# Kernel optimization log

Hardware: AMD Instinct MI355X
Metric: run time of the kernel (lower is better)

The kernel has to match this reference:

```python
import jax, jax.numpy as jnp
import numpy as np

B, N, C, HEADS, R = 8, 4096, 256, 8, 4  # N = H*W, R = reduction_ratio
LN_EPS = 1e-5


def setup_inputs() -> dict:
    key = jax.random.key(0)
    ks = jax.random.split(key, 6)
    sc = 0.02
    return {
        "x": jax.random.normal(ks[0], (B, N, C), jnp.float32),
        "conv_w": jax.random.normal(ks[1], (C, C, R, R), jnp.float32) * sc,  # OIHW
        "conv_b": jnp.zeros((C,), jnp.float32),
        "ln_g": jnp.ones((C,), jnp.float32),
        "ln_b": jnp.zeros((C,), jnp.float32),
        "kv_w": jax.random.normal(ks[2], (2 * C, C), jnp.float32) * sc,  # torch Linear (out,in)
        "kv_b": jnp.zeros((2 * C,), jnp.float32),
        "q_w": jax.random.normal(ks[3], (C, C), jnp.float32) * sc,
        "q_b": jnp.zeros((C,), jnp.float32),
        "out_w": jax.random.normal(ks[4], (C, C), jnp.float32) * sc,
        "out_b": jnp.zeros((C,), jnp.float32),
        "H": 64,
        "W": 64,
    }


def reference(x, conv_w, conv_b, ln_g, ln_b, kv_w, kv_b, q_w, q_b, out_w, out_b, H, W):
    Bz, Nq, Ch = x.shape
    d = Ch // HEADS
    scale = 1.0 / np.sqrt(float(d)).astype(np.float32)

    # spatial reduction: (B,N,C) -> (B,C,H,W) -> strided conv -> (B, M, C)
    x1 = x.transpose(0, 2, 1).reshape(Bz, Ch, H, W)
    x1 = jax.lax.conv_general_dilated(
        x1, conv_w, window_strides=(R, R), padding="VALID",
        dimension_numbers=("NCHW", "OIHW", "NCHW"))
    x1 = x1 + conv_b[None, :, None, None]
    x1 = x1.reshape(Bz, Ch, -1).transpose(0, 2, 1)  # (B, M, C), M=(H/R)*(W/R)

    # LayerNorm over channels
    mu = x1.mean(-1, keepdims=True)
    var = x1.var(-1, keepdims=True)
    x1 = (x1 - mu) / jnp.sqrt(var + LN_EPS) * ln_g + ln_b

    # K,V from reduced tokens
    kv = x1 @ kv_w.T + kv_b                                  # (B, M, 2C)
    M = kv.shape[1]
    kv = kv.reshape(Bz, M, 2, HEADS, d).transpose(2, 0, 3, 1, 4)  # (2,B,h,M,d)
    k, v = kv[0], kv[1]

    # Q from full-resolution tokens
    q = (x @ q_w.T + q_b).reshape(Bz, Nq, HEADS, d).transpose(0, 2, 1, 3)  # (B,h,N,d)

    attn = jax.nn.softmax(jnp.einsum("bhnd,bhmd->bhnm", q, k) * scale, axis=-1)
    out = jnp.einsum("bhnm,bhmd->bhnd", attn, v)             # (B,h,N,d)
    out = out.transpose(0, 2, 1, 3).reshape(Bz, Nq, Ch)
    return out @ out_w.T + out_b
```

## Files before the change

### kernel.cpp

```cpp
#include <hip/hip_runtime.h>
#include <math.h>

#define LN_EPS 1e-5f
#define SCALE_QK 0.17677669529663687f

using bf16x8 = __bf16 __attribute__((ext_vector_type(8)));
using f32x4 = float __attribute__((ext_vector_type(4)));

__device__ __forceinline__ ushort f2bf(float f) {
  unsigned u = __float_as_uint(f);
  u += 0x7fff + ((u >> 16) & 1);
  return (ushort)(u >> 16);
}

__device__ __forceinline__ void gload_lds16(const ushort* g, ushort* l) {
  __builtin_amdgcn_global_load_lds((__attribute__((address_space(1))) void*)g,
                                   (__attribute__((address_space(3))) void*)l, 16, 0, 0);
}

__global__ __launch_bounds__(256) void cast_bf16_kernel(const float* __restrict__ in,
                                                        ushort* __restrict__ out, int n4) {
  int i = blockIdx.x * 256 + threadIdx.x;
  int stride = gridDim.x * 256;
  for (; i < n4; i += stride) {
    float4 v = ((const float4*)in)[i];
    ushort4 o = {f2bf(v.x), f2bf(v.y), f2bf(v.z), f2bf(v.w)};
    ((ushort4*)out)[i] = o;
  }
}

__global__ __launch_bounds__(256) void prep_kernel(
    const float* __restrict__ qw, const float* __restrict__ kvw,
    const float* __restrict__ ow, const float* __restrict__ cw,
    ushort* __restrict__ qwb, ushort* __restrict__ kvwb,
    ushort* __restrict__ owb, ushort* __restrict__ wTb) {
  int blk = blockIdx.x, tid = threadIdx.x;
  if (blk < 256) {
    const float* src;
    ushort* dst;
    int i;
    if (blk < 64) { src = qw; dst = qwb; i = blk * 256 + tid; }
    else if (blk < 192) { src = kvw; dst = kvwb; i = (blk - 64) * 256 + tid; }
    else { src = ow; dst = owb; i = (blk - 192) * 256 + tid; }
    float4 v = ((const float4*)src)[i];
    ushort4 o = {f2bf(v.x), f2bf(v.y), f2bf(v.z), f2bf(v.w)};
    ((ushort4*)dst)[i] = o;
  } else {
    int oc = blk - 256, ic = tid;
    const float* src = cw + (size_t)oc * 4096 + ic * 16;
#pragma unroll
    for (int pos = 0; pos < 16; ++pos)
      wTb[(size_t)oc * 4096 + pos * 256 + ic] = f2bf(src[pos]);
  }
}

template <bool CONV, bool BIAS, int OUTMODE>
__global__ __launch_bounds__(256) void mfma_gemm(const ushort* __restrict__ A,
                                                 const ushort* __restrict__ Bw,
                                                 const float* __restrict__ bias,
                                                 float* __restrict__ C,
                                                 ushort* __restrict__ aux,
                                                 ushort* __restrict__ aux2, int Kld,
                                                 int Kslice, int Nld, size_t zstride) {
  __shared__ __attribute__((aligned(16))) ushort As[128 * 32];
  __shared__ __attribute__((aligned(16))) ushort Bs[64 * 32];
  int tid = threadIdx.x;
  int lane = tid & 63, w = tid >> 6;
  int m0 = blockIdx.y * 128, n0 = blockIdx.x * 64;
  int kbase = blockIdx.z * Kslice;
  int arow0 = w * 16 + (lane >> 2);
  int acol = (lane & 3) * 8;
  f32x4 acc[2][4];
#pragma unroll
  for (int i = 0; i < 2; ++i)
#pragma unroll
    for (int j = 0; j < 4; ++j) acc[i][j] = (f32x4){0.f, 0.f, 0.f, 0.f};

  for (int k0 = 0; k0 < Kslice; k0 += 32) {
    int kg = kbase + k0;
    __syncthreads();
#pragma unroll
    for (int t = 0; t < 2; ++t) {
      int row = arow0 + t * 64;
      const ushort* src;
      if (CONV) {
        int m = m0 + row;
        int b = m >> 8, mm = m & 255;
        int oh = mm >> 4, ow = mm & 15;
        int k = kg + acol;
        int pos = k >> 8, ic = k & 255;
        int n = ((oh << 2) + (pos >> 2)) * 64 + (ow << 2) + (pos & 3);
        src = A + ((size_t)(b * 4096 + n) * 256 + ic);
      } else {
        src = A + ((size_t)(m0 + row) * Kld + kg + acol);
      }
      gload_lds16(src, &As[t * 2048 + w * 512]);
    }
    {
      const ushort* srcb = Bw + ((size_t)(n0 + w * 16 + (lane >> 2)) * Kld + kg + acol);
      gload_lds16(srcb, &Bs[w * 512]);
    }
    __syncthreads();
    int qk = (lane >> 4) * 8, l15 = lane & 15;
    bf16x8 a0 = *(const bf16x8*)&As[(w * 32 + l15) * 32 + qk];
    bf16x8 a1 = *(const bf16x8*)&As[(w * 32 + 16 + l15) * 32 + qk];
#pragma unroll
    for (int j = 0; j < 4; ++j) {
      bf16x8 bj = *(const bf16x8*)&Bs[(j * 16 + l15) * 32 + qk];
      acc[0][j] = __builtin_amdgcn_mfma_f32_16x16x32_bf16(a0, bj, acc[0][j], 0, 0, 0);
      acc[1][j] = __builtin_amdgcn_mfma_f32_16x16x32_bf16(a1, bj, acc[1][j], 0, 0, 0);
    }
  }
  int l15 = lane & 15, q = lane >> 4;
  if (OUTMODE == 0) {
    float* Cz = C + (size_t)blockIdx.z * zstride;
#pragma unroll
    for (int i = 0; i < 2; ++i) {
#pragma unroll
      for (int j = 0; j < 4; ++j) {
        int col = n0 + j * 16 + l15;
        float bv = BIAS ? bias[col] : 0.f;
#pragma unroll
        for (int r = 0; r < 4; ++r) {
          int row = m0 + w * 32 + i * 16 + q * 4 + r;
          Cz[(size_t)row * Nld + col] = acc[i][j][r] + bv;
        }
      }
    }
  } else if (OUTMODE == 1) {
#pragma unroll
    for (int i = 0; i < 2; ++i) {
#pragma unroll
      for (int j = 0; j < 4; ++j) {
        int col = n0 + j * 16 + l15;
        float bv = bias[col];
#pragma unroll
        for (int r = 0; r < 4; ++r) {
          int row = m0 + w * 32 + i * 16 + q * 4 + r;
          aux[(size_t)row * Nld + col] = f2bf(acc[i][j][r] + bv);
        }
      }
    }
  } else {
#pragma unroll
    for (int i = 0; i < 2; ++i) {
      int rowb = m0 + w * 32 + i * 16 + q * 4;
      int b = rowb >> 8, mloc = rowb & 255;
#pragma unroll
      for (int j = 0; j < 4; ++j) {
        int col = n0 + j * 16 + l15;
        float bv = bias[col];
        if (col < 256) {
#pragma unroll
          for (int r = 0; r < 4; ++r)
            aux[(size_t)(b * 256 + mloc + r) * 256 + col] = f2bf(acc[i][j][r] + bv);
        } else {
          int c2 = col - 256, h = c2 >> 5, d = c2 & 31;
          unsigned lo = (unsigned)f2bf(acc[i][j][0] + bv) |
                        ((unsigned)f2bf(acc[i][j][1] + bv) << 16);
          unsigned hi = (unsigned)f2bf(acc[i][j][2] + bv) |
                        ((unsigned)f2bf(acc[i][j][3] + bv) << 16);
          *(uint2*)(aux2 + ((size_t)((b * 8 + h) * 32 + d) * 256 + mloc)) =
              make_uint2(lo, hi);
        }
      }
    }
  }
}

__global__ __launch_bounds__(256) void ln_fused(const float* __restrict__ part,
                                                const float* __restrict__ cb,
                                                const float* __restrict__ g,
                                                const float* __restrict__ bt,
                                                ushort* __restrict__ x1b) {
  int t = blockIdx.x, c = threadIdx.x;
  size_t idx = (size_t)t * 256 + c;
  float v = part[idx] + part[idx + 524288] + part[idx + 2 * 524288] +
            part[idx + 3 * 524288] + cb[c];
  float s1 = v, s2 = v * v;
#pragma unroll
  for (int o = 32; o > 0; o >>= 1) {
    s1 += __shfl_down(s1, o, 64);
    s2 += __shfl_down(s2, o, 64);
  }
  __shared__ float r1[4], r2[4];
  __shared__ float mu_s, rstd_s;
  int wv = c >> 6, lane = c & 63;
  if (lane == 0) { r1[wv] = s1; r2[wv] = s2; }
  __syncthreads();
  if (c == 0) {
    float S1 = r1[0] + r1[1] + r1[2] + r1[3];
    float S2 = r2[0] + r2[1] + r2[2] + r2[3];
    float mu = S1 * (1.f / 256.f);
    float var = S2 * (1.f / 256.f) - mu * mu;
    mu_s = mu;
    rstd_s = rsqrtf(var + LN_EPS);
  }
  __syncthreads();
  x1b[idx] = f2bf((v - mu_s) * rstd_s * g[c] + bt[c]);
}

__global__ __launch_bounds__(256) void attn_mfma(const ushort* __restrict__ qbb,
                                                 const ushort* __restrict__ kb,
                                                 const ushort* __restrict__ vT,
                                                 ushort* __restrict__ aob) {
  __shared__ __attribute__((aligned(16))) ushort P[4][16 * 264];
  int bid = blockIdx.x;
  int chunk = bid & 15, h = (bid >> 4) & 7, b = bid >> 7;
  int tid = threadIdx.x, lane = tid & 63, w = tid >> 6;
  int l15 = lane & 15, quad = lane >> 4;
  ushort* Pw = &P[w][0];

  bf16x8 kf[16];
  const ushort* kbase = kb + ((size_t)(b * 256 + l15)) * 256 + h * 32 + quad * 8;
#pragma unroll
  for (int mt = 0; mt < 16; ++mt)
    kf[mt] = *(const bf16x8*)(kbase + (size_t)mt * 16 * 256);
  bf16x8 vf[2][8];
  const ushort* vbase = vT + (size_t)(b * 8 + h) * 32 * 256;
#pragma unroll
  for (int j = 0; j < 2; ++j)
#pragma unroll
    for (int kc = 0; kc < 8; ++kc)
      vf[j][kc] = *(const bf16x8*)(vbase + (size_t)(j * 16 + l15) * 256 + kc * 32 + quad * 8);

  const float Cc = SCALE_QK * 1.4426950408889634f;
  int q0base = b * 4096 + chunk * 256 + w * 64;

  for (int t = 0; t < 4; ++t) {
    int q0 = q0base + t * 16;
    bf16x8 qf = *(const bf16x8*)(qbb + (size_t)(q0 + l15) * 256 + h * 32 + quad * 8);
    float lsum = 0.f;
#pragma unroll
    for (int mt = 0; mt < 16; ++mt) {
      f32x4 st = __builtin_amdgcn_mfma_f32_16x16x32_bf16(
          kf[mt], qf, (f32x4){0.f, 0.f, 0.f, 0.f}, 0, 0, 0);
      unsigned u[4];
#pragma unroll
      for (int r = 0; r < 4; ++r) {
        float e = exp2f(st[r] * Cc);
        unsigned ur = (__float_as_uint(e) + 0x8000u) & 0xffff0000u;
        lsum += __uint_as_float(ur);
        u[r] = ur;
      }
      unsigned lo = (u[0] >> 16) | u[1];
      unsigned hi = (u[2] >> 16) | u[3];
      *(uint2*)(Pw + l15 * 264 + mt * 16 + quad * 4) = make_uint2(lo, hi);
    }
    lsum += __shfl_xor(lsum, 16, 64);
    lsum += __shfl_xor(lsum, 32, 64);
    __threadfence_block();
    f32x4 oacc[2] = {{0.f, 0.f, 0.f, 0.f}, {0.f, 0.f, 0.f, 0.f}};
#pragma unroll
    for (int kc = 0; kc < 8; ++kc) {
      bf16x8 pf = *(const bf16x8*)(Pw + l15 * 264 + kc * 32 + quad * 8);
      oacc[0] = __builtin_amdgcn_mfma_f32_16x16x32_bf16(pf, vf[0][kc], oacc[0], 0, 0, 0);
      oacc[1] = __builtin_amdgcn_mfma_f32_16x16x32_bf16(pf, vf[1][kc], oacc[1], 0, 0, 0);
    }
    float linv[4];
#pragma unroll
    for (int r = 0; r < 4; ++r) linv[r] = 1.0f / __shfl(lsum, quad * 4 + r, 64);
    ushort* ob = aob + (size_t)q0 * 256 + h * 32;
#pragma unroll
    for (int j = 0; j < 2; ++j)
#pragma unroll
      for (int r = 0; r < 4; ++r) {
        unsigned uo = __float_as_uint(oacc[j][r] * linv[r]) + 0x8000u;
        ob[(size_t)(quad * 4 + r) * 256 + j * 16 + l15] = (ushort)(uo >> 16);
      }
  }
}

extern "C" void kernel_launch(void* const* d_in, const int* in_sizes, int n_in,
                              void* d_out, int out_size, void* d_ws, size_t ws_size,
                              hipStream_t stream) {
  const float* x = (const float*)d_in[0];
  const float* conv_w = (const float*)d_in[1];
  const float* conv_b = (const float*)d_in[2];
  const float* ln_g = (const float*)d_in[3];
  const float* ln_b = (const float*)d_in[4];
  const float* kv_w = (const float*)d_in[5];
  const float* kv_b = (const float*)d_in[6];
  const float* q_w = (const float*)d_in[7];
  const float* q_b = (const float*)d_in[8];
  const float* out_w = (const float*)d_in[9];
  const float* out_b = (const float*)d_in[10];

  ushort* xb = (ushort*)d_ws;
  ushort* wTb = xb + 8388608;
  ushort* qwb = wTb + 1048576;
  ushort* kvwb = qwb + 65536;
  ushort* owb = kvwb + 131072;
  float* part = (float*)(owb + 65536);
  ushort* x1b = (ushort*)(part + 4 * 524288);
  ushort* kb = x1b + 524288;
  ushort* vT = kb + 524288;
  ushort* aob = xb;
  ushort* qbb = (ushort*)d_out;

  cast_bf16_kernel<<<2048, 256, 0, stream>>>(x, xb, 8388608 / 4);
  prep_kernel<<<512, 256, 0, stream>>>(q_w, kv_w, out_w, conv_w, qwb, kvwb, owb, wTb);

  mfma_gemm<true, false, 0><<<dim3(4, 16, 4), 256, 0, stream>>>(
      xb, wTb, nullptr, part, nullptr, nullptr, 4096, 1024, 256, 524288);
  ln_fused<<<2048, 256, 0, stream>>>(part, conv_b, ln_g, ln_b, x1b);
  mfma_gemm<false, true, 2><<<dim3(8, 16, 1), 256, 0, stream>>>(
      x1b, kvwb, kv_b, nullptr, kb, vT, 256, 256, 512, 0);
  mfma_gemm<false, true, 1><<<dim3(4, 256, 1), 256, 0, stream>>>(
      xb, qwb, q_b, nullptr, qbb, nullptr, 256, 256, 256, 0);
  attn_mfma<<<1024, 256, 0, stream>>>(qbb, kb, vT, aob);
  mfma_gemm<false, true, 0><<<dim3(4, 256, 1), 256, 0, stream>>>(
      aob, owb, out_b, (float*)d_out, nullptr, nullptr, 256, 256, 256, 0);
}
```

Baseline: 215.2 us.

## Fuse x cast into prep, register-resident B GEMMs, deeper conv split-K, q prefetch

Merges the input cast kernel into the weight prep kernel, which saves one launch. The Q and output projections move to a new GEMM that keeps the whole 64-column weight slice in registers and reads A straight from global memory, with no LDS staging. The conv GEMM split-K goes from 4 to 8 slices, and the LayerNorm kernel now sums 8 partials. The conv partials and the bf16 q buffer are placed in the output buffer instead of the workspace, and the attention kernel prefetches the next q fragment. The risks are register pressure in the new GEMM, uncached global A reads, and extra partial-sum traffic.

```diff
diff --git a/kernel.cpp b/kernel.cpp
--- a/kernel.cpp
+++ b/kernel.cpp
@@ -18,35 +18,34 @@
                                    (__attribute__((address_space(3))) void*)l, 16, 0, 0);
 }
 
-__global__ __launch_bounds__(256) void cast_bf16_kernel(const float* __restrict__ in,
-                                                        ushort* __restrict__ out, int n4) {
-  int i = blockIdx.x * 256 + threadIdx.x;
-  int stride = gridDim.x * 256;
-  for (; i < n4; i += stride) {
-    float4 v = ((const float4*)in)[i];
-    ushort4 o = {f2bf(v.x), f2bf(v.y), f2bf(v.z), f2bf(v.w)};
-    ((ushort4*)out)[i] = o;
-  }
-}
-
 __global__ __launch_bounds__(256) void prep_kernel(
+    const float* __restrict__ x, ushort* __restrict__ xb,
     const float* __restrict__ qw, const float* __restrict__ kvw,
     const float* __restrict__ ow, const float* __restrict__ cw,
     ushort* __restrict__ qwb, ushort* __restrict__ kvwb,
     ushort* __restrict__ owb, ushort* __restrict__ wTb) {
   int blk = blockIdx.x, tid = threadIdx.x;
-  if (blk < 256) {
+  if (blk < 2048) {
+    int i = blk * 1024 + tid;
+#pragma unroll
+    for (int p = 0; p < 4; ++p) {
+      float4 v = ((const float4*)x)[i + p * 256];
+      ushort4 o = {f2bf(v.x), f2bf(v.y), f2bf(v.z), f2bf(v.w)};
+      ((ushort4*)xb)[i + p * 256] = o;
+    }
+  } else if (blk < 2304) {
+    int b2 = blk - 2048;
     const float* src;
     ushort* dst;
     int i;
-    if (blk < 64) { src = qw; dst = qwb; i = blk * 256 + tid; }
-    else if (blk < 192) { src = kvw; dst = kvwb; i = (blk - 64) * 256 + tid; }
-    else { src = ow; dst = owb; i = (blk - 192) * 256 + tid; }
+    if (b2 < 64) { src = qw; dst = qwb; i = b2 * 256 + tid; }
+    else if (b2 < 192) { src = kvw; dst = kvwb; i = (b2 - 64) * 256 + tid; }
+    else { src = ow; dst = owb; i = (b2 - 192) * 256 + tid; }
     float4 v = ((const float4*)src)[i];
     ushort4 o = {f2bf(v.x), f2bf(v.y), f2bf(v.z), f2bf(v.w)};
     ((ushort4*)dst)[i] = o;
   } else {
-    int oc = blk - 256, ic = tid;
+    int oc = blk - 2304, ic = tid;
     const float* src = cw + (size_t)oc * 4096 + ic * 16;
 #pragma unroll
     for (int pos = 0; pos < 16; ++pos)
@@ -127,20 +126,6 @@
         }
       }
     }
-  } else if (OUTMODE == 1) {
-#pragma unroll
-    for (int i = 0; i < 2; ++i) {
-#pragma unroll
-      for (int j = 0; j < 4; ++j) {
-        int col = n0 + j * 16 + l15;
-        float bv = bias[col];
-#pragma unroll
-        for (int r = 0; r < 4; ++r) {
-          int row = m0 + w * 32 + i * 16 + q * 4 + r;
-          aux[(size_t)row * Nld + col] = f2bf(acc[i][j][r] + bv);
-        }
-      }
-    }
   } else {
 #pragma unroll
     for (int i = 0; i < 2; ++i) {
@@ -168,6 +153,54 @@
   }
 }
 
+template <bool F32OUT>
+__global__ __launch_bounds__(256, 2) void breg_gemm(const ushort* __restrict__ A,
+                                                    const ushort* __restrict__ Bw,
+                                                    const float* __restrict__ bias,
+                                                    float* __restrict__ Cf,
+                                                    ushort* __restrict__ Cb) {
+  int tid = threadIdx.x, lane = tid & 63, w = tid >> 6;
+  int l15 = lane & 15, quad = lane >> 4;
+  int n0 = blockIdx.x * 64;
+  int m0 = blockIdx.y * 256 + w * 64;
+  bf16x8 bfr[4][8];
+  const ushort* bbase = Bw + (size_t)(n0 + l15) * 256 + quad * 8;
+#pragma unroll
+  for (int j = 0; j < 4; ++j)
+#pragma unroll
+    for (int kc = 0; kc < 8; ++kc)
+      bfr[j][kc] = *(const bf16x8*)(bbase + (size_t)j * 16 * 256 + kc * 32);
+  float bv[4];
+#pragma unroll
+  for (int j = 0; j < 4; ++j) bv[j] = bias[n0 + j * 16 + l15];
+
+#pragma unroll
+  for (int t = 0; t < 4; ++t) {
+    const ushort* arow = A + (size_t)(m0 + t * 16 + l15) * 256 + quad * 8;
+    bf16x8 af[8];
+#pragma unroll
+    for (int kc = 0; kc < 8; ++kc) af[kc] = *(const bf16x8*)(arow + kc * 32);
+    f32x4 acc[4];
+#pragma unroll
+    for (int j = 0; j < 4; ++j) acc[j] = (f32x4){0.f, 0.f, 0.f, 0.f};
+#pragma unroll
+    for (int kc = 0; kc < 8; ++kc)
+#pragma unroll
+      for (int j = 0; j < 4; ++j)
+        acc[j] = __builtin_amdgcn_mfma_f32_16x16x32_bf16(af[kc], bfr[j][kc], acc[j], 0, 0, 0);
+#pragma unroll
+    for (int j = 0; j < 4; ++j)
+#pragma unroll
+      for (int r = 0; r < 4; ++r) {
+        int row = m0 + t * 16 + quad * 4 + r;
+        int col = n0 + j * 16 + l15;
+        float vv = acc[j][r] + bv[j];
+        if (F32OUT) Cf[(size_t)row * 256 + col] = vv;
+        else Cb[(size_t)row * 256 + col] = f2bf(vv);
+      }
+  }
+}
+
 __global__ __launch_bounds__(256) void ln_fused(const float* __restrict__ part,
                                                 const float* __restrict__ cb,
                                                 const float* __restrict__ g,
@@ -175,8 +208,9 @@
                                                 ushort* __restrict__ x1b) {
   int t = blockIdx.x, c = threadIdx.x;
   size_t idx = (size_t)t * 256 + c;
-  float v = part[idx] + part[idx + 524288] + part[idx + 2 * 524288] +
-            part[idx + 3 * 524288] + cb[c];
+  float v = cb[c];
+#pragma unroll
+  for (int z = 0; z < 8; ++z) v += part[idx + (size_t)z * 524288];
   float s1 = v, s2 = v * v;
 #pragma unroll
   for (int o = 32; o > 0; o >>= 1) {
@@ -226,10 +260,13 @@
 
   const float Cc = SCALE_QK * 1.4426950408889634f;
   int q0base = b * 4096 + chunk * 256 + w * 64;
-
+  const ushort* qptr = qbb + (size_t)(q0base + l15) * 256 + h * 32 + quad * 8;
+
+  bf16x8 qn = *(const bf16x8*)qptr;
   for (int t = 0; t < 4; ++t) {
+    bf16x8 qf = qn;
+    if (t < 3) qn = *(const bf16x8*)(qptr + (size_t)(t + 1) * 16 * 256);
     int q0 = q0base + t * 16;
-    bf16x8 qf = *(const bf16x8*)(qbb + (size_t)(q0 + l15) * 256 + h * 32 + quad * 8);
     float lsum = 0.f;
 #pragma unroll
     for (int mt = 0; mt < 16; ++mt) {
@@ -291,24 +328,21 @@
   ushort* qwb = wTb + 1048576;
   ushort* kvwb = qwb + 65536;
   ushort* owb = kvwb + 131072;
-  float* part = (float*)(owb + 65536);
-  ushort* x1b = (ushort*)(part + 4 * 524288);
+  ushort* x1b = owb + 65536;
   ushort* kb = x1b + 524288;
   ushort* vT = kb + 524288;
   ushort* aob = xb;
-  ushort* qbb = (ushort*)d_out;
-
-  cast_bf16_kernel<<<2048, 256, 0, stream>>>(x, xb, 8388608 / 4);
-  prep_kernel<<<512, 256, 0, stream>>>(q_w, kv_w, out_w, conv_w, qwb, kvwb, owb, wTb);
-
-  mfma_gemm<true, false, 0><<<dim3(4, 16, 4), 256, 0, stream>>>(
-      xb, wTb, nullptr, part, nullptr, nullptr, 4096, 1024, 256, 524288);
+  float* part = (float*)d_out;
+  ushort* qbb = (ushort*)((float*)d_out + 4194304);
+
+  prep_kernel<<<2560, 256, 0, stream>>>(x, xb, q_w, kv_w, out_w, conv_w,
+                                        qwb, kvwb, owb, wTb);
+  mfma_gemm<true, false, 0><<<dim3(4, 16, 8), 256, 0, stream>>>(
+      xb, wTb, nullptr, part, nullptr, nullptr, 4096, 512, 256, 524288);
   ln_fused<<<2048, 256, 0, stream>>>(part, conv_b, ln_g, ln_b, x1b);
   mfma_gemm<false, true, 2><<<dim3(8, 16, 1), 256, 0, stream>>>(
       x1b, kvwb, kv_b, nullptr, kb, vT, 256, 256, 512, 0);
-  mfma_gemm<false, true, 1><<<dim3(4, 256, 1), 256, 0, stream>>>(
-      xb, qwb, q_b, nullptr, qbb, nullptr, 256, 256, 256, 0);
+  breg_gemm<false><<<dim3(4, 128), 256, 0, stream>>>(xb, qwb, q_b, nullptr, qbb);
   attn_mfma<<<1024, 256, 0, stream>>>(qbb, kb, vT, aob);
-  mfma_gemm<false, true, 0><<<dim3(4, 256, 1), 256, 0, stream>>>(
-      aob, owb, out_b, (float*)d_out, nullptr, nullptr, 256, 256, 256, 0);
-}
+  breg_gemm<true><<<dim3(4, 128), 256, 0, stream>>>(aob, owb, out_b, (float*)d_out, nullptr);
+}
```

Result: no change. 216.7 us (+0.7%).
